# Kernel tuning notes

Measured on AMD Instinct MI355X. Metric: run time of the kernel, lower is better.

Reference implementation:

```python
import jax, jax.numpy as jnp
import numpy as np


def setup_inputs() -> dict:
    key = jax.random.key(0)
    ks = jax.random.split(key, 5)
    B, S, D, H, DK = 2, 2048, 1024, 16, 64
    scale = 1.0 / np.sqrt(D)
    return {
        "x": jax.random.normal(ks[0], (B, S, D), dtype=jnp.float32),
        "Wq": jax.random.normal(ks[1], (H, D, DK), dtype=jnp.float32) * scale,
        "Wk": jax.random.normal(ks[2], (H, D, DK), dtype=jnp.float32) * scale,
        "Wv": jax.random.normal(ks[3], (H, D, DK), dtype=jnp.float32) * scale,
        "Wo": jax.random.normal(ks[4], (D, D), dtype=jnp.float32) * scale,
    }


def reference(x, Wq, Wk, Wv, Wo):
    # x: (B, S, D); Wq/Wk/Wv: (H, D, d_k); Wo: (D, D) torch-Linear convention (y = c @ Wo.T)
    B, S, D = x.shape
    H, _, dk = Wq.shape
    Q = jnp.einsum('bsd,hdk->bhsk', x, Wq)  # (B,H,S,dk)
    K = jnp.einsum('bsd,hdk->bhsk', x, Wk)
    V = jnp.einsum('bsd,hdk->bhsk', x, Wv)
    scores = jnp.einsum('bhqk,bhsk->bhqs', Q, K) / jnp.sqrt(jnp.float32(dk))  # (B,H,S,S)
    causal = jnp.tril(jnp.ones((S, S), dtype=bool))
    scores = jnp.where(causal[None, None, :, :], scores, -jnp.inf)
    weights = jax.nn.softmax(scores, axis=-1)
    out = jnp.einsum('bhqs,bhsk->bhqk', weights, V)  # (B,H,S,dk)
    concat = out.transpose(0, 2, 1, 3).reshape(B, S, H * dk)  # heads concatenated h-major
    return concat @ Wo.T
```

## Files before the change

### kernel.cpp

```cpp
#include <hip/hip_runtime.h>

typedef unsigned short u16;
typedef unsigned int u32;
typedef __bf16 bf16x8 __attribute__((ext_vector_type(8)));
typedef float f32x4 __attribute__((ext_vector_type(4)));
typedef u16 u16x8 __attribute__((ext_vector_type(8)));
typedef u16 u16x4 __attribute__((ext_vector_type(4)));
typedef u32 u32x4 __attribute__((ext_vector_type(4)));

#define NH 16
#define DKK 64
#define SQ 2048
#define DD 1024

#define AS1 __attribute__((address_space(1)))
#define AS3 __attribute__((address_space(3)))

#define QSCALE 0.1803368925f

__device__ inline u16 f2bf(float f) {
  union { float f; u32 u; } v; v.f = f;
  u32 u = v.u;
  u += 0x7FFFu + ((u >> 16) & 1u);
  return (u16)(u >> 16);
}

__device__ __forceinline__ u32 cvtpk(float lo, float hi) {
  u32 r;
  asm("v_cvt_pk_bf16_f32 %0, %1, %2" : "=v"(r) : "v"(lo), "v"(hi));
  return r;
}

__device__ inline u16x8 cvt8(const float* p) {
  float4 a = *(const float4*)p;
  float4 b = *(const float4*)(p + 4);
  u16x8 v;
  v[0] = f2bf(a.x); v[1] = f2bf(a.y); v[2] = f2bf(a.z); v[3] = f2bf(a.w);
  v[4] = f2bf(b.x); v[5] = f2bf(b.y); v[6] = f2bf(b.z); v[7] = f2bf(b.w);
  return v;
}

__device__ __forceinline__ void gload16(const u16* g, u16* l) {
  __builtin_amdgcn_global_load_lds((const AS1 u32*)(const void*)g,
                                   (AS3 u32*)(void*)l, 16, 0, 0);
}

__global__ __launch_bounds__(256) void prep_kernel(const float* __restrict__ x,
                                                   u16* __restrict__ xb,
                                                   const float* __restrict__ Wo,
                                                   u16* __restrict__ Wob,
                                                   const float* __restrict__ Wq,
                                                   const float* __restrict__ Wk,
                                                   const float* __restrict__ Wv,
                                                   u16* __restrict__ WT) {
  __shared__ u16 sm[64][72];
  int bid = blockIdx.x;
  int tid = threadIdx.x;
  if (bid < 2560) {
    const float* src; u16* dst; size_t base;
    if (bid < 2048) { src = x;  dst = xb;  base = (size_t)bid * 2048; }
    else            { src = Wo; dst = Wob; base = (size_t)(bid - 2048) * 2048; }
    size_t off = base + (size_t)tid * 8;
    *(u16x8*)&dst[off] = cvt8(&src[off]);
    return;
  }
  int wid = bid - 2560;
  int t = wid >> 8;
  int rem = wid & 255;
  int h = rem >> 4;
  int d0 = (rem & 15) * 64;
  const float* src = (t == 0) ? Wq : (t == 1) ? Wk : Wv;
  for (int j = 0; j < 2; ++j) {
    int idx = tid + j * 256;
    int r = idx >> 3;
    int c0 = (idx & 7) * 8;
    *(u16x8*)&sm[r][c0] = cvt8(&src[(h * DD + d0 + r) * DKK + c0]);
  }
  __syncthreads();
  for (int j = 0; j < 2; ++j) {
    int idx = tid + j * 256;
    int r2 = idx >> 3;
    int c0 = (idx & 7) * 8;
    u16x8 vv;
    for (int i = 0; i < 8; ++i) vv[i] = sm[c0 + i][r2];
    int n = t * 1024 + h * 64 + r2;
    *(u16x8*)&WT[n * DD + d0 + c0] = vv;
  }
}

__global__ __launch_bounds__(256) void gemm128(const u16* __restrict__ A,
                                               const u16* __restrict__ Bm,
                                               int mode,
                                               u16* __restrict__ o0,
                                               u16* __restrict__ o1,
                                               u16* __restrict__ o2,
                                               float* __restrict__ of) {
  __shared__ u16 As[128 * 64];
  __shared__ u16 Bs[128 * 64];
  const int K = 1024;
  int m0 = blockIdx.x * 128;
  int n0 = blockIdx.y * 128;
  int tid = threadIdx.x;
  int w = tid >> 6, l = tid & 63;
  int lg = l >> 4, lr = l & 15;
  int wr = w >> 1, wc = w & 1;

  int srow = w * 32 + (l >> 3);
  int sg = (l & 7) ^ ((l >> 3) & 7);
  const u16* gA = A + (size_t)(m0 + srow) * K + sg * 8;
  const u16* gB = Bm + (size_t)(n0 + srow) * K + sg * 8;
  u16* lA = As + (w * 32) * 64;
  u16* lB = Bs + (w * 32) * 64;
  int key = lr & 7;

  f32x4 acc[4][4] = {};
  for (int kt = 0; kt < 16; ++kt) {
    int k0 = kt * 64;
    #pragma unroll
    for (int g = 0; g < 4; ++g) {
      gload16(gA + k0 + g * 8 * K, lA + g * 8 * 64);
      gload16(gB + k0 + g * 8 * K, lB + g * 8 * 64);
    }
    __syncthreads();
    #pragma unroll
    for (int kk = 0; kk < 2; ++kk) {
      bf16x8 a[4], b[4];
      #pragma unroll
      for (int m = 0; m < 4; ++m)
        a[m] = *(const bf16x8*)&As[(wr * 64 + m * 16 + lr) * 64 + (((kk * 4 + lg) ^ key) * 8)];
      #pragma unroll
      for (int n = 0; n < 4; ++n)
        b[n] = *(const bf16x8*)&Bs[(wc * 64 + n * 16 + lr) * 64 + (((kk * 4 + lg) ^ key) * 8)];
      #pragma unroll
      for (int m = 0; m < 4; ++m)
        #pragma unroll
        for (int n = 0; n < 4; ++n)
          acc[m][n] = __builtin_amdgcn_mfma_f32_16x16x32_bf16(a[m], b[n], acc[m][n], 0, 0, 0);
    }
    __syncthreads();
  }

  if (mode == 1) {
    int mbase = m0 + wr * 64 + lg * 4;
    int nbase = n0 + wc * 64 + lr;
    #pragma unroll
    for (int m = 0; m < 4; ++m)
      #pragma unroll
      for (int n = 0; n < 4; ++n)
        #pragma unroll
        for (int rr = 0; rr < 4; ++rr)
          of[(size_t)(mbase + m * 16 + rr) * 1024 + nbase + n * 16] = acc[m][n][rr];
  } else {
    int t = n0 >> 10;
    int h = (((n0 & 1023) + wc * 64) >> 6);
    int bq = m0 >> 11;
    int sbase = (m0 & 2047) + wr * 64 + lg * 4;
    if (t < 2) {
      float sc = (t == 0) ? QSCALE : 1.0f;
      u16* o = (t == 0) ? o0 : o1;
      u16* op = o + (size_t)(bq * NH + h) * SQ * DKK;
      #pragma unroll
      for (int m = 0; m < 4; ++m)
        #pragma unroll
        for (int n = 0; n < 4; ++n)
          #pragma unroll
          for (int rr = 0; rr < 4; ++rr)
            op[(size_t)(sbase + m * 16 + rr) * DKK + n * 16 + lr] = f2bf(acc[m][n][rr] * sc);
    } else {
      u16* op = o2 + (size_t)(bq * NH + h) * DKK * SQ;
      int Sb = (m0 & 2047) + wr * 64;
      #pragma unroll
      for (int m = 0; m < 4; ++m)
        #pragma unroll
        for (int n = 0; n < 4; ++n) {
          u16x4 vv;
          #pragma unroll
          for (int rr = 0; rr < 4; ++rr) vv[rr] = f2bf(acc[m][n][rr]);
          *(u16x4*)&op[(size_t)(n * 16 + lr) * SQ + Sb + (m >> 1) * 32 + lg * 8 + (m & 1) * 4] = vv;
        }
    }
  }
}

__global__ __launch_bounds__(256) void attn_kernel(const u16* __restrict__ Q,
                                                   const u16* __restrict__ Kg,
                                                   const u16* __restrict__ Vt,
                                                   u16* __restrict__ Cc) {
  __shared__ u16 Ks[2][64 * 64];
  __shared__ u16 Vs[2][64 * 64];
  int bh = blockIdx.x;
  int y = blockIdx.y;
  int a = y & 7, bsel = y >> 3;
  int s = (bsel == 0) ? 2 * a : (bsel == 1) ? 2 * a + 1
        : (bsel == 2) ? 30 - 2 * a : 31 - 2 * a;
  int tid = threadIdx.x;
  int w = tid >> 6, l = tid & 63;
  int lg = l >> 4, lr = l & 15;
  const u16* Qp = Q + (size_t)bh * SQ * DKK;
  const u16* Kp = Kg + (size_t)bh * SQ * DKK;
  const u16* Vp = Vt + (size_t)bh * DKK * SQ;
  int b = bh >> 4, h = bh & 15;
  int cur = 0;

  int lrow8 = l >> 3;
  int swz = (l & 7) ^ lrow8;
  int r7 = lr & 7;
  const u16* kSrc0 = Kp + (size_t)(w * 16 + lrow8) * DKK + swz * 8;
  const u16* kSrc1 = Kp + (size_t)(w * 16 + 8 + lrow8) * DKK + swz * 8;
  const u16* vSrc0 = Vp + (size_t)(w * 16 + lrow8) * SQ + swz * 8;
  const u16* vSrc1 = Vp + (size_t)(w * 16 + 8 + lrow8) * SQ + swz * 8;

  #define STAGE(buf, j0)                                                  \
    do {                                                                  \
      gload16(kSrc0 + (size_t)(j0) * DKK, &Ks[buf][(w * 16) * 64]);       \
      gload16(kSrc1 + (size_t)(j0) * DKK, &Ks[buf][(w * 16 + 8) * 64]);   \
      gload16(vSrc0 + (j0), &Vs[buf][(w * 16) * 64]);                     \
      gload16(vSrc1 + (j0), &Vs[buf][(w * 16 + 8) * 64]);                 \
    } while (0)

  STAGE(0, 0);
  __syncthreads();

  int qrow = s * 64 + w * 16 + lr;
  bf16x8 qf0 = *(const bf16x8*)&Qp[(size_t)qrow * DKK + lg * 8];
  bf16x8 qf1 = *(const bf16x8*)&Qp[(size_t)qrow * DKK + 32 + lg * 8];
  f32x4 o[4] = {};
  float mrun = -1e30f, lpart = 0.f;

  for (int jt = 0; jt <= s; ++jt) {
    if (jt < s) STAGE(cur ^ 1, (jt + 1) * 64);

    float p[16];
    __builtin_amdgcn_s_setprio(1);
    #pragma unroll
    for (int c = 0; c < 4; ++c) {
      int R = c * 16 + lr;
      const u16* kr = &Ks[cur][R * 64];
      bf16x8 k0 = *(const bf16x8*)&kr[(lg ^ r7) * 8];
      bf16x8 k1 = *(const bf16x8*)&kr[((4 + lg) ^ r7) * 8];
      f32x4 z = {};
      z = __builtin_amdgcn_mfma_f32_16x16x32_bf16(k0, qf0, z, 0, 0, 0);
      z = __builtin_amdgcn_mfma_f32_16x16x32_bf16(k1, qf1, z, 0, 0, 0);
      #pragma unroll
      for (int rr = 0; rr < 4; ++rr) p[c * 4 + rr] = z[rr];
    }
    __builtin_amdgcn_s_setprio(0);
    if (jt == s) {
      int j0 = jt * 64;
      #pragma unroll
      for (int c = 0; c < 4; ++c)
        #pragma unroll
        for (int rr = 0; rr < 4; ++rr) {
          int kv = j0 + c * 16 + lg * 4 + rr;
          if (kv > qrow) p[c * 4 + rr] = -1e30f;
        }
    }
    float t0 = fmaxf(fmaxf(p[0], p[1]), p[2]);
    float t1 = fmaxf(fmaxf(p[3], p[4]), p[5]);
    float t2 = fmaxf(fmaxf(p[6], p[7]), p[8]);
    float t3 = fmaxf(fmaxf(p[9], p[10]), p[11]);
    float t4 = fmaxf(fmaxf(p[12], p[13]), p[14]);
    float pm = fmaxf(fmaxf(fmaxf(t0, t1), fmaxf(t2, t3)), fmaxf(t4, p[15]));
    pm = fmaxf(pm, __shfl_xor(pm, 16, 64));
    pm = fmaxf(pm, __shfl_xor(pm, 32, 64));
    if (__any(pm > mrun + 11.0f)) {
      float mnew = fmaxf(mrun, pm);
      float alpha = exp2f(mrun - mnew);
      mrun = mnew;
      lpart *= alpha;
      float af[4];
      #pragma unroll
      for (int rr = 0; rr < 4; ++rr) af[rr] = __shfl(alpha, lg * 4 + rr, 64);
      #pragma unroll
      for (int n = 0; n < 4; ++n)
        #pragma unroll
        for (int rr = 0; rr < 4; ++rr) o[n][rr] *= af[rr];
    }
    float su = 0.f;
    #pragma unroll
    for (int i = 0; i < 16; ++i) { p[i] = exp2f(p[i] - mrun); su += p[i]; }
    lpart += su;
    union { u32x4 w; bf16x8 v; } pk0, pk1;
    pk0.w[0] = cvtpk(p[0],  p[1]);
    pk0.w[1] = cvtpk(p[2],  p[3]);
    pk0.w[2] = cvtpk(p[4],  p[5]);
    pk0.w[3] = cvtpk(p[6],  p[7]);
    pk1.w[0] = cvtpk(p[8],  p[9]);
    pk1.w[1] = cvtpk(p[10], p[11]);
    pk1.w[2] = cvtpk(p[12], p[13]);
    pk1.w[3] = cvtpk(p[14], p[15]);
    {
      bf16x8 pa0 = pk0.v, pa1 = pk1.v;
      __builtin_amdgcn_s_setprio(1);
      #pragma unroll
      for (int n = 0; n < 4; ++n) {
        int R2 = n * 16 + lr;
        bf16x8 vb0 = *(const bf16x8*)&Vs[cur][R2 * 64 + ((lg ^ r7) * 8)];
        o[n] = __builtin_amdgcn_mfma_f32_16x16x32_bf16(pa0, vb0, o[n], 0, 0, 0);
        bf16x8 vb1 = *(const bf16x8*)&Vs[cur][R2 * 64 + (((4 + lg) ^ r7) * 8)];
        o[n] = __builtin_amdgcn_mfma_f32_16x16x32_bf16(pa1, vb1, o[n], 0, 0, 0);
      }
      __builtin_amdgcn_s_setprio(0);
    }
    __syncthreads();
    cur ^= 1;
  }

  float lsum = lpart;
  lsum += __shfl_xor(lsum, 16, 64);
  lsum += __shfl_xor(lsum, 32, 64);
  float lrow[4];
  #pragma unroll
  for (int rr = 0; rr < 4; ++rr) lrow[rr] = __shfl(lsum, lg * 4 + rr, 64);
  int srow = s * 64 + w * 16 + lg * 4;
  #pragma unroll
  for (int n = 0; n < 4; ++n)
    #pragma unroll
    for (int rr = 0; rr < 4; ++rr) {
      float val = o[n][rr] / lrow[rr];
      Cc[((size_t)(b * SQ + srow + rr)) * DD + h * DKK + n * 16 + lr] = f2bf(val);
    }
  #undef STAGE
}

extern "C" void kernel_launch(void* const* d_in, const int* in_sizes, int n_in,
                              void* d_out, int out_size, void* d_ws, size_t ws_size,
                              hipStream_t stream) {
  (void)in_sizes; (void)n_in; (void)out_size; (void)ws_size;
  const float* x  = (const float*)d_in[0];
  const float* Wq = (const float*)d_in[1];
  const float* Wk = (const float*)d_in[2];
  const float* Wv = (const float*)d_in[3];
  const float* Wo = (const float*)d_in[4];
  float* out = (float*)d_out;
  u16* ws = (u16*)d_ws;
  u16* WT  = ws;
  u16* Qb  = WT + 3145728;
  u16* Kb  = Qb + 4194304;
  u16* Vb  = Kb + 4194304;
  u16* XC  = Vb + 4194304;
  u16* Wob = XC + 4194304;

  hipLaunchKernelGGL(prep_kernel, dim3(3328), dim3(256), 0, stream, x, XC, Wo, Wob, Wq, Wk, Wv, WT);
  hipLaunchKernelGGL(gemm128, dim3(32, 24), dim3(256), 0, stream, XC, WT, 0, Qb, Kb, Vb, (float*)nullptr);
  hipLaunchKernelGGL(attn_kernel, dim3(32, 32), dim3(256), 0, stream, Qb, Kb, Vb, XC);
  hipLaunchKernelGGL(gemm128, dim3(32, 8), dim3(256), 0, stream, XC, Wob, 1, nullptr, nullptr, nullptr, out);
}
```

Before: 123.1 us.

## Split long causal attention rows into two KV chunks with a combine pass

```diff
diff --git a/kernel.cpp b/kernel.cpp
--- a/kernel.cpp
+++ b/kernel.cpp
@@ -18,11 +18,26 @@
 
 #define QSCALE 0.1803368925f
 
+__constant__ int TS[48]  = {15,30,31,31,28,27,12,24, 29,29,30,14,22,25,26,10,
+                            27,28,13,26,21,25,21,20, 23,23,24,11,19,16,18,22,
+                            16, 6, 5, 4,17,18,19,20,  0, 1, 2, 3,17, 7, 8, 9};
+__constant__ int TT0[48] = { 0,15, 0,16,14, 0, 0,12,  0,15, 0, 0,11, 0, 0, 0,
+                            14, 0, 0,13, 0,13,11,10,  0,12, 0, 0, 0, 8, 9, 0,
+                             0, 0, 0, 0, 0, 0,10, 0,  0, 0, 0, 0, 9, 0, 0, 0};
+__constant__ int TNT[48] = {16,16,16,16,15,14,13,13, 15,15,15,15,12,13,13,11,
+                            14,14,14,14,11,13,11,11, 12,12,12,12,10, 9,10,11,
+                             8, 7, 6, 5, 9, 9,10,10,  1, 2, 3, 4, 9, 8, 9,10};
+
 __device__ inline u16 f2bf(float f) {
   union { float f; u32 u; } v; v.f = f;
   u32 u = v.u;
   u += 0x7FFFu + ((u >> 16) & 1u);
   return (u16)(u >> 16);
+}
+
+__device__ inline float bf2f(u16 x) {
+  union { u32 u; float f; } v; v.u = ((u32)x) << 16;
+  return v.f;
 }
 
 __device__ __forceinline__ u32 cvtpk(float lo, float hi) {
@@ -185,14 +200,18 @@
 __global__ __launch_bounds__(256) void attn_kernel(const u16* __restrict__ Q,
                                                    const u16* __restrict__ Kg,
                                                    const u16* __restrict__ Vt,
-                                                   u16* __restrict__ Cc) {
+                                                   u16* __restrict__ Cc,
+                                                   u16* __restrict__ oP,
+                                                   float* __restrict__ mP,
+                                                   float* __restrict__ lP) {
   __shared__ u16 Ks[2][64 * 64];
   __shared__ u16 Vs[2][64 * 64];
   int bh = blockIdx.x;
   int y = blockIdx.y;
-  int a = y & 7, bsel = y >> 3;
-  int s = (bsel == 0) ? 2 * a : (bsel == 1) ? 2 * a + 1
-        : (bsel == 2) ? 30 - 2 * a : 31 - 2 * a;
+  int s = TS[y], t0 = TT0[y], nt = TNT[y];
+  int send = t0 + nt - 1;
+  bool partial = (s >= 16);
+  bool masked = (send == s);
   int tid = threadIdx.x;
   int w = tid >> 6, l = tid & 63;
   int lg = l >> 4, lr = l & 15;
@@ -218,7 +237,7 @@
       gload16(vSrc1 + (j0), &Vs[buf][(w * 16 + 8) * 64]);                 \
     } while (0)
 
-  STAGE(0, 0);
+  STAGE(0, t0 * 64);
   __syncthreads();
 
   int qrow = s * 64 + w * 16 + lr;
@@ -227,8 +246,8 @@
   f32x4 o[4] = {};
   float mrun = -1e30f, lpart = 0.f;
 
-  for (int jt = 0; jt <= s; ++jt) {
-    if (jt < s) STAGE(cur ^ 1, (jt + 1) * 64);
+  for (int jt = t0; jt <= send; ++jt) {
+    if (jt < send) STAGE(cur ^ 1, (jt + 1) * 64);
 
     float p[16];
     __builtin_amdgcn_s_setprio(1);
@@ -245,7 +264,7 @@
       for (int rr = 0; rr < 4; ++rr) p[c * 4 + rr] = z[rr];
     }
     __builtin_amdgcn_s_setprio(0);
-    if (jt == s) {
+    if (masked && jt == s) {
       int j0 = jt * 64;
       #pragma unroll
       for (int c = 0; c < 4; ++c)
@@ -255,12 +274,12 @@
           if (kv > qrow) p[c * 4 + rr] = -1e30f;
         }
     }
-    float t0 = fmaxf(fmaxf(p[0], p[1]), p[2]);
-    float t1 = fmaxf(fmaxf(p[3], p[4]), p[5]);
-    float t2 = fmaxf(fmaxf(p[6], p[7]), p[8]);
-    float t3 = fmaxf(fmaxf(p[9], p[10]), p[11]);
-    float t4 = fmaxf(fmaxf(p[12], p[13]), p[14]);
-    float pm = fmaxf(fmaxf(fmaxf(t0, t1), fmaxf(t2, t3)), fmaxf(t4, p[15]));
+    float t0m = fmaxf(fmaxf(p[0], p[1]), p[2]);
+    float t1m = fmaxf(fmaxf(p[3], p[4]), p[5]);
+    float t2m = fmaxf(fmaxf(p[6], p[7]), p[8]);
+    float t3m = fmaxf(fmaxf(p[9], p[10]), p[11]);
+    float t4m = fmaxf(fmaxf(p[12], p[13]), p[14]);
+    float pm = fmaxf(fmaxf(fmaxf(t0m, t1m), fmaxf(t2m, t3m)), fmaxf(t4m, p[15]));
     pm = fmaxf(pm, __shfl_xor(pm, 16, 64));
     pm = fmaxf(pm, __shfl_xor(pm, 32, 64));
     if (__any(pm > mrun + 11.0f)) {
@@ -309,18 +328,66 @@
   float lsum = lpart;
   lsum += __shfl_xor(lsum, 16, 64);
   lsum += __shfl_xor(lsum, 32, 64);
-  float lrow[4];
+  if (!partial) {
+    float lrow[4];
+    #pragma unroll
+    for (int rr = 0; rr < 4; ++rr) lrow[rr] = __shfl(lsum, lg * 4 + rr, 64);
+    int srow = s * 64 + w * 16 + lg * 4;
+    #pragma unroll
+    for (int n = 0; n < 4; ++n)
+      #pragma unroll
+      for (int rr = 0; rr < 4; ++rr) {
+        float val = o[n][rr] / lrow[rr];
+        Cc[((size_t)(b * SQ + srow + rr)) * DD + h * DKK + n * 16 + lr] = f2bf(val);
+      }
+  } else {
+    int half = (t0 != 0) ? 1 : 0;
+    size_t cb = ((size_t)(bh * 16 + (s - 16)) * 2 + half);
+    u16* op = oP + cb * 4096;
+    #pragma unroll
+    for (int n = 0; n < 4; ++n)
+      #pragma unroll
+      for (int rr = 0; rr < 4; ++rr)
+        op[(w * 16 + lg * 4 + rr) * 64 + n * 16 + lr] = f2bf(o[n][rr]);
+    if (lg == 0) {
+      mP[cb * 64 + w * 16 + lr] = mrun;
+      lP[cb * 64 + w * 16 + lr] = lsum;
+    }
+  }
+  #undef STAGE
+}
+
+__global__ __launch_bounds__(256) void combine_kernel(const u16* __restrict__ oP,
+                                                      const float* __restrict__ mP,
+                                                      const float* __restrict__ lP,
+                                                      u16* __restrict__ Cc) {
+  int bh = blockIdx.x;
+  int ss = blockIdx.y;
+  int tid = threadIdx.x;
+  int row = tid >> 2;
+  int c0 = (tid & 3) * 16;
+  size_t base = (size_t)(bh * 16 + ss) * 2;
+  float mA = mP[base * 64 + row],       mB = mP[(base + 1) * 64 + row];
+  float lA = lP[base * 64 + row],       lB = lP[(base + 1) * 64 + row];
+  float m = fmaxf(mA, mB);
+  float eA = exp2f(mA - m), eB = exp2f(mB - m);
+  float inv = 1.0f / (lA * eA + lB * eB);
+  float sA = eA * inv, sB = eB * inv;
+  const u16* pA = oP + base * 4096 + row * 64 + c0;
+  const u16* pB = oP + (base + 1) * 4096 + row * 64 + c0;
+  int s = ss + 16;
+  int b = bh >> 4, h = bh & 15;
+  u16* dst = Cc + ((size_t)(b * SQ + s * 64 + row)) * DD + h * DKK + c0;
+  u16x8 a0 = *(const u16x8*)pA, a1 = *(const u16x8*)(pA + 8);
+  u16x8 b0 = *(const u16x8*)pB, b1 = *(const u16x8*)(pB + 8);
+  u16x8 r0, r1;
   #pragma unroll
-  for (int rr = 0; rr < 4; ++rr) lrow[rr] = __shfl(lsum, lg * 4 + rr, 64);
-  int srow = s * 64 + w * 16 + lg * 4;
-  #pragma unroll
-  for (int n = 0; n < 4; ++n)
-    #pragma unroll
-    for (int rr = 0; rr < 4; ++rr) {
-      float val = o[n][rr] / lrow[rr];
-      Cc[((size_t)(b * SQ + srow + rr)) * DD + h * DKK + n * 16 + lr] = f2bf(val);
-    }
-  #undef STAGE
+  for (int i = 0; i < 8; ++i) {
+    r0[i] = f2bf(bf2f(a0[i]) * sA + bf2f(b0[i]) * sB);
+    r1[i] = f2bf(bf2f(a1[i]) * sA + bf2f(b1[i]) * sB);
+  }
+  *(u16x8*)dst = r0;
+  *(u16x8*)(dst + 8) = r1;
 }
 
 extern "C" void kernel_launch(void* const* d_in, const int* in_sizes, int n_in,
@@ -340,9 +407,13 @@
   u16* Vb  = Kb + 4194304;
   u16* XC  = Vb + 4194304;
   u16* Wob = XC + 4194304;
+  u16* oP  = Wob + 1048576;
+  float* mP = (float*)(oP + 4194304);
+  float* lP = mP + 65536;
 
   hipLaunchKernelGGL(prep_kernel, dim3(3328), dim3(256), 0, stream, x, XC, Wo, Wob, Wq, Wk, Wv, WT);
   hipLaunchKernelGGL(gemm128, dim3(32, 24), dim3(256), 0, stream, XC, WT, 0, Qb, Kb, Vb, (float*)nullptr);
-  hipLaunchKernelGGL(attn_kernel, dim3(32, 32), dim3(256), 0, stream, Qb, Kb, Vb, XC);
+  hipLaunchKernelGGL(attn_kernel, dim3(32, 48), dim3(256), 0, stream, Qb, Kb, Vb, XC, oP, mP, lP);
+  hipLaunchKernelGGL(combine_kernel, dim3(32, 16), dim3(256), 0, stream, oP, mP, lP, XC);
   hipLaunchKernelGGL(gemm128, dim3(32, 8), dim3(256), 0, stream, XC, Wob, 1, nullptr, nullptr, nullptr, out);
 }
```

Result: no change. 124.9 us (+1.5%).
